# Performance work log

Hardware: AMD Instinct MI355X
Metric: run time of the kernel (lower is better)

## Reference

```python
import jax, jax.numpy as jnp
import numpy as np

LOG_STD_MAX = 2.0
LOG_STD_MIN = -5.0
HEIGHT = 4          # tree height -> 16 leaves, 15 internal nodes
TOP_K = 4           # top-k leaves kept in soft gate
SMAX_TEMP = 1.0     # softmax temperature over selected leaf logits


def _path_matrix(height: int) -> np.ndarray:
    """[N_internal, L] matrix with +1 where a leaf's root-to-leaf path goes
    left through a node, -1 where it goes right, 0 otherwise."""
    L = 2 ** height
    P = np.zeros((L - 1, L), dtype=np.float32)
    for leaf in range(L):
        node = 0
        for lvl in range(height):
            bit = (leaf >> (height - 1 - lvl)) & 1
            P[node, leaf] = 1.0 if bit == 0 else -1.0
            node = 2 * node + 1 + bit
    return P


def setup_inputs() -> dict:
    key = jax.random.key(0)
    k0, k1, k2, k3, k4 = jax.random.split(key, 5)
    B, D, A = 262144, 128, 8
    L = 2 ** HEIGHT
    N = L - 1
    x = jax.random.normal(k0, (B, D), dtype=jnp.float32)
    Wn = jax.random.normal(k1, (D, N), dtype=jnp.float32) / np.float32(np.sqrt(D))
    bn = jax.random.normal(k2, (N,), dtype=jnp.float32) * 0.01
    Wl = jax.random.normal(k3, (L, D, 2 * A), dtype=jnp.float32) / np.float32(np.sqrt(D))
    bl = jax.random.normal(k4, (L, 2 * A), dtype=jnp.float32) * 0.01
    return {"x": x, "Wn": Wn, "bn": bn, "Wl": Wl, "bl": bl}


def reference(x, Wn, bn, Wl, bl):
    L = Wl.shape[0]
    P = jnp.asarray(_path_matrix(HEIGHT))              # [N, L] constant

    # --- differentiable-tree routing ---
    node_logits = x @ Wn + bn                          # [B, N]
    leaf_logits = node_logits @ P                      # [B, L]
    vals, idx = jax.lax.top_k(leaf_logits, TOP_K)      # [B, k]
    soft = jax.nn.softmax(vals / SMAX_TEMP, axis=-1)   # [B, k]
    onehot = jax.nn.one_hot(idx, L, dtype=x.dtype)     # [B, k, L]
    gate_soft = jnp.einsum('bk,bkl->bl', soft, onehot) # scatter soft weights
    gate_hard = onehot[:, 0]                           # argmax leaf one-hot
    # hard argmax forward, top-k softmax gradient (straight-through)
    gate = gate_hard + gate_soft - jax.lax.stop_gradient(gate_soft)

    # --- per-leaf linear controllers, gated sum ---
    leaf_out = jnp.einsum('bd,ldo->blo', x, Wl) + bl   # [B, L, 2A]
    out = jnp.einsum('bl,blo->bo', gate, leaf_out)     # [B, 2A]

    A = out.shape[-1] // 2
    mean, log_std = out[:, :A], out[:, A:]
    log_std = jnp.tanh(log_std)
    log_std = LOG_STD_MIN + 0.5 * (LOG_STD_MAX - LOG_STD_MIN) * (log_std + 1.0)
    return mean, log_std
```

## Files before the change

kernel.cpp:

```cpp
#include <hip/hip_runtime.h>
#include <math.h>

#define BLK  256
#define DD   128
#define NN   15
#define NL   16
#define OC   16
#define WSTR 260

__global__ __launch_bounds__(BLK, 6)
void dts_fused4(const float* __restrict__ x, const float* __restrict__ Wn,
                const float* __restrict__ bn, const float* __restrict__ Wl,
                const float* __restrict__ bl, float* __restrict__ out, int B)
{
    __shared__ __align__(16) float sWnT[NN * DD];
    __shared__ __align__(16) float sWl[NL * WSTR];
    __shared__ float sBn[NN];
    __shared__ __align__(16) float sBl[NL * OC];

    const int t = threadIdx.x;
    const int row = blockIdx.x * BLK + t;
    const int rowL = (row < B) ? row : 0;
    const float4* xr = reinterpret_cast<const float4*>(x + (size_t)rowL * DD);

    for (int i = t; i < NN * DD; i += BLK) {
        int n = i >> 7, d = i & 127;
        sWnT[i] = Wn[d * NN + n];
    }
    if (t < NN) sBn[t] = bn[t];
    for (int i = t; i < NL * OC; i += BLK) sBl[i] = bl[i];
    __syncthreads();

    float acc[NN];
    #pragma unroll
    for (int n = 0; n < NN; ++n) acc[n] = 0.f;
    #pragma unroll 4
    for (int q = 0; q < DD / 4; ++q) {
        const float4 xv = xr[q];
        #pragma unroll
        for (int n = 0; n < NN; ++n) {
            const float4 w = *(const float4*)&sWnT[n * DD + q * 4];
            acc[n] = fmaf(xv.w, w.w, fmaf(xv.z, w.z,
                     fmaf(xv.y, w.y, fmaf(xv.x, w.x, acc[n]))));
        }
    }
    #pragma unroll
    for (int n = 0; n < NN; ++n) acc[n] += sBn[n];

    float L2a[4], L3a[8], L4a[16];
    {
        float p = acc[0], m = -acc[0];
        L2a[0] = p + acc[1]; L2a[1] = p - acc[1];
        L2a[2] = m + acc[2]; L2a[3] = m - acc[2];
        #pragma unroll
        for (int i = 0; i < 4; ++i) { L3a[2*i] = L2a[i] + acc[3+i]; L3a[2*i+1] = L2a[i] - acc[3+i]; }
        #pragma unroll
        for (int i = 0; i < 8; ++i) { L4a[2*i] = L3a[i] + acc[7+i]; L4a[2*i+1] = L3a[i] - acc[7+i]; }
    }
    int best = 0; float bv = L4a[0];
    #pragma unroll
    for (int l = 1; l < NL; ++l) if (L4a[l] > bv) { bv = L4a[l]; best = l; }

    float4 o0, o1, o2, o3;
    {
        const float4* blv = reinterpret_cast<const float4*>(&sBl[best * OC]);
        o0 = blv[0]; o1 = blv[1]; o2 = blv[2]; o3 = blv[3];
    }
    const int wlofs = best * WSTR;

    const float* gw = Wl + ((size_t)(t >> 4) * (DD * OC) + (t & 15) * 16);
    const int stofs = (t >> 4) * WSTR + (t & 15) * 16;

    #pragma unroll 1
    for (int c = 0; c < 8; ++c) {
        const float* g_ = gw + c * 256;
        const float4 s0 = *(const float4*)(g_);
        const float4 s1 = *(const float4*)(g_ + 4);
        const float4 s2 = *(const float4*)(g_ + 8);
        const float4 s3 = *(const float4*)(g_ + 12);

        __syncthreads();
        {
            float* d_ = &sWl[stofs];
            *(float4*)(d_)      = s0; *(float4*)(d_ + 4)  = s1;
            *(float4*)(d_ + 8)  = s2; *(float4*)(d_ + 12) = s3;
        }
        __syncthreads();

        const float4 xc0 = xr[c * 4 + 0];
        const float4 xc1 = xr[c * 4 + 1];
        const float4 xc2 = xr[c * 4 + 2];
        const float4 xc3 = xr[c * 4 + 3];

        const float* wb = &sWl[wlofs];
        #define KSTEP(xv, k) { \
            const float4 w0 = *(const float4*)&wb[(k) * 16 + 0];  \
            const float4 w1 = *(const float4*)&wb[(k) * 16 + 4];  \
            const float4 w2 = *(const float4*)&wb[(k) * 16 + 8];  \
            const float4 w3 = *(const float4*)&wb[(k) * 16 + 12]; \
            o0.x = fmaf((xv), w0.x, o0.x); o0.y = fmaf((xv), w0.y, o0.y); \
            o0.z = fmaf((xv), w0.z, o0.z); o0.w = fmaf((xv), w0.w, o0.w); \
            o1.x = fmaf((xv), w1.x, o1.x); o1.y = fmaf((xv), w1.y, o1.y); \
            o1.z = fmaf((xv), w1.z, o1.z); o1.w = fmaf((xv), w1.w, o1.w); \
            o2.x = fmaf((xv), w2.x, o2.x); o2.y = fmaf((xv), w2.y, o2.y); \
            o2.z = fmaf((xv), w2.z, o2.z); o2.w = fmaf((xv), w2.w, o2.w); \
            o3.x = fmaf((xv), w3.x, o3.x); o3.y = fmaf((xv), w3.y, o3.y); \
            o3.z = fmaf((xv), w3.z, o3.z); o3.w = fmaf((xv), w3.w, o3.w); }
        KSTEP(xc0.x,  0) KSTEP(xc0.y,  1) KSTEP(xc0.z,  2) KSTEP(xc0.w,  3)
        KSTEP(xc1.x,  4) KSTEP(xc1.y,  5) KSTEP(xc1.z,  6) KSTEP(xc1.w,  7)
        KSTEP(xc2.x,  8) KSTEP(xc2.y,  9) KSTEP(xc2.z, 10) KSTEP(xc2.w, 11)
        KSTEP(xc3.x, 12) KSTEP(xc3.y, 13) KSTEP(xc3.z, 14) KSTEP(xc3.w, 15)
        #undef KSTEP
    }

    if (row < B) {
        size_t ob = (size_t)row * 8;
        *reinterpret_cast<float4*>(&out[ob])     = o0;
        *reinterpret_cast<float4*>(&out[ob + 4]) = o1;

        float4 r0, r1;
        #define SQ(v) (-1.5f + 3.5f * (1.f - 2.f / (__expf(2.f * (v)) + 1.f)))
        r0.x = SQ(o2.x); r0.y = SQ(o2.y); r0.z = SQ(o2.z); r0.w = SQ(o2.w);
        r1.x = SQ(o3.x); r1.y = SQ(o3.y); r1.z = SQ(o3.z); r1.w = SQ(o3.w);
        #undef SQ
        size_t ob2 = (size_t)B * 8 + ob;
        *reinterpret_cast<float4*>(&out[ob2])     = r0;
        *reinterpret_cast<float4*>(&out[ob2 + 4]) = r1;
    }
}

extern "C" void kernel_launch(void* const* d_in, const int* in_sizes, int n_in,
                              void* d_out, int out_size, void* d_ws, size_t ws_size,
                              hipStream_t stream)
{
    const float* x  = (const float*)d_in[0];
    const float* Wn = (const float*)d_in[1];
    const float* bn = (const float*)d_in[2];
    const float* Wl = (const float*)d_in[3];
    const float* bl = (const float*)d_in[4];
    float* out = (float*)d_out;

    const int B = in_sizes[0] / DD;
    const int blocks = (B + BLK - 1) / BLK;

    hipLaunchKernelGGL(dts_fused4, dim3(blocks), dim3(BLK), 0, stream,
                       x, Wn, bn, Wl, bl, out, B);
}
```

Measured before the change: 71.03 us.

## Sort block rows by selected leaf to make leaf-weight LDS reads uniform

Inside each block, threads bin their rows by argmax leaf using a shared histogram, a prefix scan and a permutation. Each thread then processes the permuted row, reading that row's x chunks through shared memory, so neighbouring lanes mostly share a leaf and its weight reads become broadcasts instead of scattered bank-conflicting accesses. Results are un-permuted through shared memory before the tanh epilogue and the store. The cost is extra barriers, extra LDS traffic for x and the outputs, the launch-bounds occupancy hint dropping from 6 to 4, and float4 LDS accesses at a 17-float stride that are not 16-byte aligned.

```diff
diff --git a/kernel.cpp b/kernel.cpp
--- a/kernel.cpp
+++ b/kernel.cpp
@@ -7,16 +7,21 @@
 #define NL   16
 #define OC   16
 #define WSTR 260
+#define XSTR 17
 
-__global__ __launch_bounds__(BLK, 6)
-void dts_fused4(const float* __restrict__ x, const float* __restrict__ Wn,
+__global__ __launch_bounds__(BLK, 4)
+void dts_fused5(const float* __restrict__ x, const float* __restrict__ Wn,
                 const float* __restrict__ bn, const float* __restrict__ Wl,
                 const float* __restrict__ bl, float* __restrict__ out, int B)
 {
-    __shared__ __align__(16) float sWnT[NN * DD];
+    __shared__ __align__(16) float uShared[BLK * XSTR];
     __shared__ __align__(16) float sWl[NL * WSTR];
     __shared__ float sBn[NN];
     __shared__ __align__(16) float sBl[NL * OC];
+    __shared__ int sPerm[BLK];
+    __shared__ int sLeaf[BLK];
+    __shared__ int sBins[NL];
+    __shared__ int sStarts[NL];
 
     const int t = threadIdx.x;
     const int row = blockIdx.x * BLK + t;
@@ -25,10 +30,11 @@
 
     for (int i = t; i < NN * DD; i += BLK) {
         int n = i >> 7, d = i & 127;
-        sWnT[i] = Wn[d * NN + n];
+        uShared[i] = Wn[d * NN + n];
     }
     if (t < NN) sBn[t] = bn[t];
     for (int i = t; i < NL * OC; i += BLK) sBl[i] = bl[i];
+    if (t < NL) sBins[t] = 0;
     __syncthreads();
 
     float acc[NN];
@@ -39,7 +45,7 @@
         const float4 xv = xr[q];
         #pragma unroll
         for (int n = 0; n < NN; ++n) {
-            const float4 w = *(const float4*)&sWnT[n * DD + q * 4];
+            const float4 w = *(const float4*)&uShared[n * DD + q * 4];
             acc[n] = fmaf(xv.w, w.w, fmaf(xv.z, w.z,
                      fmaf(xv.y, w.y, fmaf(xv.x, w.x, acc[n]))));
         }
@@ -61,12 +67,32 @@
     #pragma unroll
     for (int l = 1; l < NL; ++l) if (L4a[l] > bv) { bv = L4a[l]; best = l; }
 
+    int rank = atomicAdd(&sBins[best], 1);
+    __syncthreads();
+    if (t == 0) {
+        int s = 0;
+        #pragma unroll
+        for (int l = 0; l < NL; ++l) { sStarts[l] = s; s += sBins[l]; }
+    }
+    __syncthreads();
+    {
+        int slot = sStarts[best] + rank;
+        sPerm[slot] = t;
+        sLeaf[slot] = best;
+    }
+    __syncthreads();
+
+    const int r    = sPerm[t];
+    const int leaf = sLeaf[t];
+    const float* wb = &sWl[leaf * WSTR];
+    float* xmine = &uShared[t * XSTR];
+    const float* xperm = &uShared[r * XSTR];
+
     float4 o0, o1, o2, o3;
     {
-        const float4* blv = reinterpret_cast<const float4*>(&sBl[best * OC]);
+        const float4* blv = reinterpret_cast<const float4*>(&sBl[leaf * OC]);
         o0 = blv[0]; o1 = blv[1]; o2 = blv[2]; o3 = blv[3];
     }
-    const int wlofs = best * WSTR;
 
     const float* gw = Wl + ((size_t)(t >> 4) * (DD * OC) + (t & 15) * 16);
     const int stofs = (t >> 4) * WSTR + (t & 15) * 16;
@@ -78,26 +104,34 @@
         const float4 s1 = *(const float4*)(g_ + 4);
         const float4 s2 = *(const float4*)(g_ + 8);
         const float4 s3 = *(const float4*)(g_ + 12);
+        const float4 xc0 = xr[c * 4 + 0];
+        const float4 xc1 = xr[c * 4 + 1];
+        const float4 xc2 = xr[c * 4 + 2];
+        const float4 xc3 = xr[c * 4 + 3];
 
         __syncthreads();
         {
             float* d_ = &sWl[stofs];
             *(float4*)(d_)      = s0; *(float4*)(d_ + 4)  = s1;
             *(float4*)(d_ + 8)  = s2; *(float4*)(d_ + 12) = s3;
+            *(float4*)(xmine)       = xc0;
+            *(float4*)(xmine + 4)   = xc1;
+            *(float4*)(xmine + 8)   = xc2;
+            *(float4*)(xmine + 12)  = xc3;
         }
         __syncthreads();
 
-        const float4 xc0 = xr[c * 4 + 0];
-        const float4 xc1 = xr[c * 4 + 1];
-        const float4 xc2 = xr[c * 4 + 2];
-        const float4 xc3 = xr[c * 4 + 3];
+        const float4 a0 = *(const float4*)(xperm);
+        const float4 a1 = *(const float4*)(xperm + 4);
+        const float4 a2 = *(const float4*)(xperm + 8);
+        const float4 a3 = *(const float4*)(xperm + 12);
 
-        const float* wb = &sWl[wlofs];
+        const float* wc = wb;
         #define KSTEP(xv, k) { \
-            const float4 w0 = *(const float4*)&wb[(k) * 16 + 0];  \
-            const float4 w1 = *(const float4*)&wb[(k) * 16 + 4];  \
-            const float4 w2 = *(const float4*)&wb[(k) * 16 + 8];  \
-            const float4 w3 = *(const float4*)&wb[(k) * 16 + 12]; \
+            const float4 w0 = *(const float4*)&wc[(k) * 16 + 0];  \
+            const float4 w1 = *(const float4*)&wc[(k) * 16 + 4];  \
+            const float4 w2 = *(const float4*)&wc[(k) * 16 + 8];  \
+            const float4 w3 = *(const float4*)&wc[(k) * 16 + 12]; \
             o0.x = fmaf((xv), w0.x, o0.x); o0.y = fmaf((xv), w0.y, o0.y); \
             o0.z = fmaf((xv), w0.z, o0.z); o0.w = fmaf((xv), w0.w, o0.w); \
             o1.x = fmaf((xv), w1.x, o1.x); o1.y = fmaf((xv), w1.y, o1.y); \
@@ -106,22 +140,36 @@
             o2.z = fmaf((xv), w2.z, o2.z); o2.w = fmaf((xv), w2.w, o2.w); \
             o3.x = fmaf((xv), w3.x, o3.x); o3.y = fmaf((xv), w3.y, o3.y); \
             o3.z = fmaf((xv), w3.z, o3.z); o3.w = fmaf((xv), w3.w, o3.w); }
-        KSTEP(xc0.x,  0) KSTEP(xc0.y,  1) KSTEP(xc0.z,  2) KSTEP(xc0.w,  3)
-        KSTEP(xc1.x,  4) KSTEP(xc1.y,  5) KSTEP(xc1.z,  6) KSTEP(xc1.w,  7)
-        KSTEP(xc2.x,  8) KSTEP(xc2.y,  9) KSTEP(xc2.z, 10) KSTEP(xc2.w, 11)
-        KSTEP(xc3.x, 12) KSTEP(xc3.y, 13) KSTEP(xc3.z, 14) KSTEP(xc3.w, 15)
+        KSTEP(a0.x,  0) KSTEP(a0.y,  1) KSTEP(a0.z,  2) KSTEP(a0.w,  3)
+        KSTEP(a1.x,  4) KSTEP(a1.y,  5) KSTEP(a1.z,  6) KSTEP(a1.w,  7)
+        KSTEP(a2.x,  8) KSTEP(a2.y,  9) KSTEP(a2.z, 10) KSTEP(a2.w, 11)
+        KSTEP(a3.x, 12) KSTEP(a3.y, 13) KSTEP(a3.z, 14) KSTEP(a3.w, 15)
         #undef KSTEP
     }
 
+    __syncthreads();
+    {
+        float* d_ = &uShared[r * XSTR];
+        *(float4*)(d_)      = o0; *(float4*)(d_ + 4)  = o1;
+        *(float4*)(d_ + 8)  = o2; *(float4*)(d_ + 12) = o3;
+    }
+    __syncthreads();
+
     if (row < B) {
+        const float* so = &uShared[t * XSTR];
+        const float4 m0 = *(const float4*)(so);
+        const float4 m1 = *(const float4*)(so + 4);
+        const float4 s0 = *(const float4*)(so + 8);
+        const float4 s1 = *(const float4*)(so + 12);
+
         size_t ob = (size_t)row * 8;
-        *reinterpret_cast<float4*>(&out[ob])     = o0;
-        *reinterpret_cast<float4*>(&out[ob + 4]) = o1;
+        *reinterpret_cast<float4*>(&out[ob])     = m0;
+        *reinterpret_cast<float4*>(&out[ob + 4]) = m1;
 
         float4 r0, r1;
         #define SQ(v) (-1.5f + 3.5f * (1.f - 2.f / (__expf(2.f * (v)) + 1.f)))
-        r0.x = SQ(o2.x); r0.y = SQ(o2.y); r0.z = SQ(o2.z); r0.w = SQ(o2.w);
-        r1.x = SQ(o3.x); r1.y = SQ(o3.y); r1.z = SQ(o3.z); r1.w = SQ(o3.w);
+        r0.x = SQ(s0.x); r0.y = SQ(s0.y); r0.z = SQ(s0.z); r0.w = SQ(s0.w);
+        r1.x = SQ(s1.x); r1.y = SQ(s1.y); r1.z = SQ(s1.z); r1.w = SQ(s1.w);
         #undef SQ
         size_t ob2 = (size_t)B * 8 + ob;
         *reinterpret_cast<float4*>(&out[ob2])     = r0;
@@ -143,6 +191,6 @@
     const int B = in_sizes[0] / DD;
     const int blocks = (B + BLK - 1) / BLK;
 
-    hipLaunchKernelGGL(dts_fused4, dim3(blocks), dim3(BLK), 0, stream,
+    hipLaunchKernelGGL(dts_fused5, dim3(blocks), dim3(BLK), 0, stream,
                        x, Wn, bn, Wl, bl, out, B);
 }
```

After: 97.45 us. 1.37x slower.

## Bucket rows by selected leaf and compute leaf GEMM with bf16 MFMA tiles

Applied to the files above, without the earlier changes.

After routing, rows in each block are binned by their argmax leaf using shared-memory atomics, and a tile list of 16-row groups per leaf is built. The per-leaf 128x16 linear layer then runs as bf16 MFMA 16x16x32 ops on the permuted rows, with x and Wl converted to bf16 in shared memory. This replaces the scalar FP32 FMA path with matrix-core work. It lowers precision of the leaf matmul to bf16, adds per-block sorting overhead and padded tiles, and scatters outputs as scalar stores.

```diff
diff --git a/kernel.cpp b/kernel.cpp
--- a/kernel.cpp
+++ b/kernel.cpp
@@ -6,20 +6,45 @@
 #define NN   15
 #define NL   16
 #define OC   16
-#define WSTR 260
-
-__global__ __launch_bounds__(BLK, 6)
-void dts_fused4(const float* __restrict__ x, const float* __restrict__ Wn,
+#define XROWS 272
+#define XSTR  40
+#define WSTR  40
+#define MAXT  32
+#define TPW   8
+
+typedef __attribute__((ext_vector_type(8))) short short8v;
+typedef __attribute__((ext_vector_type(4))) float f32x4;
+
+__device__ inline unsigned pack_bf16(float a, float b) {
+    unsigned ua = __float_as_uint(a); ua = (ua + 0x7FFFu + ((ua >> 16) & 1u)) >> 16;
+    unsigned ub = __float_as_uint(b); ub = (ub + 0x7FFFu + ((ub >> 16) & 1u)) >> 16;
+    return ua | (ub << 16);
+}
+
+__global__ __launch_bounds__(BLK, 3)
+void dts_fused6(const float* __restrict__ x, const float* __restrict__ Wn,
                 const float* __restrict__ bn, const float* __restrict__ Wl,
                 const float* __restrict__ bl, float* __restrict__ out, int B)
 {
     __shared__ __align__(16) float sWnT[NN * DD];
-    __shared__ __align__(16) float sWl[NL * WSTR];
+    __shared__ __align__(16) unsigned short sX[XROWS * XSTR];
+    __shared__ __align__(16) unsigned short sWT[NL * OC * WSTR];
     __shared__ float sBn[NN];
     __shared__ __align__(16) float sBl[NL * OC];
-
-    const int t = threadIdx.x;
-    const int row = blockIdx.x * BLK + t;
+    __shared__ int sPerm[BLK];
+    __shared__ int sBins[NL];
+    __shared__ int sStarts[NL];
+    __shared__ int sTleaf[MAXT];
+    __shared__ int sTm0[MAXT];
+    __shared__ int sTend[MAXT];
+    __shared__ int sNT;
+
+    const int t  = threadIdx.x;
+    const int wv = t >> 6;
+    const int lo = t & 15;
+    const int grp = (t >> 4) & 3;
+    const int rowBase = blockIdx.x * BLK;
+    const int row = rowBase + t;
     const int rowL = (row < B) ? row : 0;
     const float4* xr = reinterpret_cast<const float4*>(x + (size_t)rowL * DD);
 
@@ -29,103 +54,150 @@
     }
     if (t < NN) sBn[t] = bn[t];
     for (int i = t; i < NL * OC; i += BLK) sBl[i] = bl[i];
-    __syncthreads();
-
-    float acc[NN];
-    #pragma unroll
-    for (int n = 0; n < NN; ++n) acc[n] = 0.f;
+    if (t < NL) sBins[t] = 0;
+    __syncthreads();
+
+    float acc1[NN];
+    #pragma unroll
+    for (int n = 0; n < NN; ++n) acc1[n] = 0.f;
     #pragma unroll 4
     for (int q = 0; q < DD / 4; ++q) {
         const float4 xv = xr[q];
         #pragma unroll
         for (int n = 0; n < NN; ++n) {
             const float4 w = *(const float4*)&sWnT[n * DD + q * 4];
-            acc[n] = fmaf(xv.w, w.w, fmaf(xv.z, w.z,
-                     fmaf(xv.y, w.y, fmaf(xv.x, w.x, acc[n]))));
-        }
-    }
-    #pragma unroll
-    for (int n = 0; n < NN; ++n) acc[n] += sBn[n];
+            acc1[n] = fmaf(xv.w, w.w, fmaf(xv.z, w.z,
+                      fmaf(xv.y, w.y, fmaf(xv.x, w.x, acc1[n]))));
+        }
+    }
+    #pragma unroll
+    for (int n = 0; n < NN; ++n) acc1[n] += sBn[n];
 
     float L2a[4], L3a[8], L4a[16];
     {
-        float p = acc[0], m = -acc[0];
-        L2a[0] = p + acc[1]; L2a[1] = p - acc[1];
-        L2a[2] = m + acc[2]; L2a[3] = m - acc[2];
-        #pragma unroll
-        for (int i = 0; i < 4; ++i) { L3a[2*i] = L2a[i] + acc[3+i]; L3a[2*i+1] = L2a[i] - acc[3+i]; }
-        #pragma unroll
-        for (int i = 0; i < 8; ++i) { L4a[2*i] = L3a[i] + acc[7+i]; L4a[2*i+1] = L3a[i] - acc[7+i]; }
+        float p = acc1[0], m = -acc1[0];
+        L2a[0] = p + acc1[1]; L2a[1] = p - acc1[1];
+        L2a[2] = m + acc1[2]; L2a[3] = m - acc1[2];
+        #pragma unroll
+        for (int i = 0; i < 4; ++i) { L3a[2*i] = L2a[i] + acc1[3+i]; L3a[2*i+1] = L2a[i] - acc1[3+i]; }
+        #pragma unroll
+        for (int i = 0; i < 8; ++i) { L4a[2*i] = L3a[i] + acc1[7+i]; L4a[2*i+1] = L3a[i] - acc1[7+i]; }
     }
     int best = 0; float bv = L4a[0];
     #pragma unroll
     for (int l = 1; l < NL; ++l) if (L4a[l] > bv) { bv = L4a[l]; best = l; }
 
-    float4 o0, o1, o2, o3;
-    {
-        const float4* blv = reinterpret_cast<const float4*>(&sBl[best * OC]);
-        o0 = blv[0]; o1 = blv[1]; o2 = blv[2]; o3 = blv[3];
-    }
-    const int wlofs = best * WSTR;
-
-    const float* gw = Wl + ((size_t)(t >> 4) * (DD * OC) + (t & 15) * 16);
-    const int stofs = (t >> 4) * WSTR + (t & 15) * 16;
+    int rank = atomicAdd(&sBins[best], 1);
+    __syncthreads();
+    if (t == 0) {
+        int s = 0, nt = 0;
+        #pragma unroll
+        for (int l = 0; l < NL; ++l) {
+            sStarts[l] = s;
+            int c = sBins[l];
+            for (int m0 = s; m0 < s + c; m0 += 16) {
+                sTleaf[nt] = l; sTm0[nt] = m0; sTend[nt] = s + c; ++nt;
+            }
+            s += c;
+        }
+        sNT = nt;
+    }
+    __syncthreads();
+    const int slot = sStarts[best] + rank;
+    sPerm[slot] = t;
+    __syncthreads();
+    const int nT = sNT;
+
+    int tleaf[TPW], tm0[TPW], tend[TPW], aoff[TPW], boff[TPW];
+    #pragma unroll
+    for (int i = 0; i < TPW; ++i) {
+        int tid = wv + i * 4;
+        bool v = tid < nT;
+        tleaf[i] = v ? sTleaf[tid] : 0;
+        tm0[i]   = v ? sTm0[tid]   : 0;
+        tend[i]  = v ? sTend[tid]  : 0;
+        aoff[i]  = (tm0[i] + lo) * XSTR + grp * 8;
+        boff[i]  = tleaf[i] * (OC * WSTR) + lo * WSTR + grp * 8;
+    }
+    f32x4 accm[TPW];
+    #pragma unroll
+    for (int i = 0; i < TPW; ++i) accm[i] = (f32x4){0.f, 0.f, 0.f, 0.f};
+
+    const int kk = t & 15;
+    const int wleaf = t >> 4;
+    unsigned short* xdst = &sX[slot * XSTR];
+    unsigned short* wdst = &sWT[wleaf * (OC * WSTR) + kk * 2];
 
     #pragma unroll 1
-    for (int c = 0; c < 8; ++c) {
-        const float* g_ = gw + c * 256;
-        const float4 s0 = *(const float4*)(g_);
-        const float4 s1 = *(const float4*)(g_ + 4);
-        const float4 s2 = *(const float4*)(g_ + 8);
-        const float4 s3 = *(const float4*)(g_ + 12);
+    for (int c = 0; c < 4; ++c) {
+        const float4 x0 = xr[c*8+0], x1 = xr[c*8+1], x2 = xr[c*8+2], x3 = xr[c*8+3];
+        const float4 x4 = xr[c*8+4], x5 = xr[c*8+5], x6 = xr[c*8+6], x7 = xr[c*8+7];
+        const float* gp = Wl + (size_t)wleaf * (DD * OC) + (size_t)(c * 32 + kk * 2) * OC;
+        const float4 wa0 = *(const float4*)(gp);      const float4 wa1 = *(const float4*)(gp + 4);
+        const float4 wa2 = *(const float4*)(gp + 8);  const float4 wa3 = *(const float4*)(gp + 12);
+        const float4 wb0 = *(const float4*)(gp + 16); const float4 wb1 = *(const float4*)(gp + 20);
+        const float4 wb2 = *(const float4*)(gp + 24); const float4 wb3 = *(const float4*)(gp + 28);
 
         __syncthreads();
         {
-            float* d_ = &sWl[stofs];
-            *(float4*)(d_)      = s0; *(float4*)(d_ + 4)  = s1;
-            *(float4*)(d_ + 8)  = s2; *(float4*)(d_ + 12) = s3;
+            uint4* xd = (uint4*)xdst;
+            xd[0] = make_uint4(pack_bf16(x0.x,x0.y), pack_bf16(x0.z,x0.w),
+                               pack_bf16(x1.x,x1.y), pack_bf16(x1.z,x1.w));
+            xd[1] = make_uint4(pack_bf16(x2.x,x2.y), pack_bf16(x2.z,x2.w),
+                               pack_bf16(x3.x,x3.y), pack_bf16(x3.z,x3.w));
+            xd[2] = make_uint4(pack_bf16(x4.x,x4.y), pack_bf16(x4.z,x4.w),
+                               pack_bf16(x5.x,x5.y), pack_bf16(x5.z,x5.w));
+            xd[3] = make_uint4(pack_bf16(x6.x,x6.y), pack_bf16(x6.z,x6.w),
+                               pack_bf16(x7.x,x7.y), pack_bf16(x7.z,x7.w));
+            *(unsigned*)&wdst[ 0*WSTR] = pack_bf16(wa0.x, wb0.x);
+            *(unsigned*)&wdst[ 1*WSTR] = pack_bf16(wa0.y, wb0.y);
+            *(unsigned*)&wdst[ 2*WSTR] = pack_bf16(wa0.z, wb0.z);
+            *(unsigned*)&wdst[ 3*WSTR] = pack_bf16(wa0.w, wb0.w);
+            *(unsigned*)&wdst[ 4*WSTR] = pack_bf16(wa1.x, wb1.x);
+            *(unsigned*)&wdst[ 5*WSTR] = pack_bf16(wa1.y, wb1.y);
+            *(unsigned*)&wdst[ 6*WSTR] = pack_bf16(wa1.z, wb1.z);
+            *(unsigned*)&wdst[ 7*WSTR] = pack_bf16(wa1.w, wb1.w);
+            *(unsigned*)&wdst[ 8*WSTR] = pack_bf16(wa2.x, wb2.x);
+            *(unsigned*)&wdst[ 9*WSTR] = pack_bf16(wa2.y, wb2.y);
+            *(unsigned*)&wdst[10*WSTR] = pack_bf16(wa2.z, wb2.z);
+            *(unsigned*)&wdst[11*WSTR] = pack_bf16(wa2.w, wb2.w);
+            *(unsigned*)&wdst[12*WSTR] = pack_bf16(wa3.x, wb3.x);
+            *(unsigned*)&wdst[13*WSTR] = pack_bf16(wa3.y, wb3.y);
+            *(unsigned*)&wdst[14*WSTR] = pack_bf16(wa3.z, wb3.z);
+            *(unsigned*)&wdst[15*WSTR] = pack_bf16(wa3.w, wb3.w);
         }
         __syncthreads();
 
-        const float4 xc0 = xr[c * 4 + 0];
-        const float4 xc1 = xr[c * 4 + 1];
-        const float4 xc2 = xr[c * 4 + 2];
-        const float4 xc3 = xr[c * 4 + 3];
-
-        const float* wb = &sWl[wlofs];
-        #define KSTEP(xv, k) { \
-            const float4 w0 = *(const float4*)&wb[(k) * 16 + 0];  \
-            const float4 w1 = *(const float4*)&wb[(k) * 16 + 4];  \
-            const float4 w2 = *(const float4*)&wb[(k) * 16 + 8];  \
-            const float4 w3 = *(const float4*)&wb[(k) * 16 + 12]; \
-            o0.x = fmaf((xv), w0.x, o0.x); o0.y = fmaf((xv), w0.y, o0.y); \
-            o0.z = fmaf((xv), w0.z, o0.z); o0.w = fmaf((xv), w0.w, o0.w); \
-            o1.x = fmaf((xv), w1.x, o1.x); o1.y = fmaf((xv), w1.y, o1.y); \
-            o1.z = fmaf((xv), w1.z, o1.z); o1.w = fmaf((xv), w1.w, o1.w); \
-            o2.x = fmaf((xv), w2.x, o2.x); o2.y = fmaf((xv), w2.y, o2.y); \
-            o2.z = fmaf((xv), w2.z, o2.z); o2.w = fmaf((xv), w2.w, o2.w); \
-            o3.x = fmaf((xv), w3.x, o3.x); o3.y = fmaf((xv), w3.y, o3.y); \
-            o3.z = fmaf((xv), w3.z, o3.z); o3.w = fmaf((xv), w3.w, o3.w); }
-        KSTEP(xc0.x,  0) KSTEP(xc0.y,  1) KSTEP(xc0.z,  2) KSTEP(xc0.w,  3)
-        KSTEP(xc1.x,  4) KSTEP(xc1.y,  5) KSTEP(xc1.z,  6) KSTEP(xc1.w,  7)
-        KSTEP(xc2.x,  8) KSTEP(xc2.y,  9) KSTEP(xc2.z, 10) KSTEP(xc2.w, 11)
-        KSTEP(xc3.x, 12) KSTEP(xc3.y, 13) KSTEP(xc3.z, 14) KSTEP(xc3.w, 15)
-        #undef KSTEP
-    }
-
-    if (row < B) {
-        size_t ob = (size_t)row * 8;
-        *reinterpret_cast<float4*>(&out[ob])     = o0;
-        *reinterpret_cast<float4*>(&out[ob + 4]) = o1;
-
-        float4 r0, r1;
-        #define SQ(v) (-1.5f + 3.5f * (1.f - 2.f / (__expf(2.f * (v)) + 1.f)))
-        r0.x = SQ(o2.x); r0.y = SQ(o2.y); r0.z = SQ(o2.z); r0.w = SQ(o2.w);
-        r1.x = SQ(o3.x); r1.y = SQ(o3.y); r1.z = SQ(o3.z); r1.w = SQ(o3.w);
-        #undef SQ
-        size_t ob2 = (size_t)B * 8 + ob;
-        *reinterpret_cast<float4*>(&out[ob2])     = r0;
-        *reinterpret_cast<float4*>(&out[ob2 + 4]) = r1;
+        #pragma unroll
+        for (int i = 0; i < TPW; ++i) {
+            if (wv + i * 4 < nT) {
+                short8v af = *(const short8v*)&sX[aoff[i]];
+                short8v bf = *(const short8v*)&sWT[boff[i]];
+                accm[i] = __builtin_amdgcn_mfma_f32_16x16x32_bf16(af, bf, accm[i], 0, 0, 0);
+            }
+        }
+    }
+
+    #pragma unroll
+    for (int i = 0; i < TPW; ++i) {
+        if (wv + i * 4 < nT) {
+            const float bias = sBl[tleaf[i] * OC + lo];
+            #pragma unroll
+            for (int j = 0; j < 4; ++j) {
+                const int sl = tm0[i] + grp * 4 + j;
+                if (sl < tend[i]) {
+                    const int r = sPerm[sl];
+                    const size_t grow = (size_t)rowBase + r;
+                    const float v = accm[i][j] + bias;
+                    if (lo < 8) {
+                        out[grow * 8 + lo] = v;
+                    } else {
+                        out[(size_t)B * 8 + grow * 8 + (lo - 8)] =
+                            -1.5f + 3.5f * (1.f - 2.f / (__expf(2.f * v) + 1.f));
+                    }
+                }
+            }
+        }
     }
 }
 
@@ -143,6 +215,6 @@
     const int B = in_sizes[0] / DD;
     const int blocks = (B + BLK - 1) / BLK;
 
-    hipLaunchKernelGGL(dts_fused4, dim3(blocks), dim3(BLK), 0, stream,
+    hipLaunchKernelGGL(dts_fused6, dim3(blocks), dim3(BLK), 0, stream,
                        x, Wn, bn, Wl, bl, out, B);
 }
```

Result: slower. 89.97 us (+26.7%).
